# Kernel optimization log

Hardware: AMD Instinct MI355X
Metric: run time of the kernel (lower is better)

The kernel has to match this reference:

```python
import jax, jax.numpy as jnp
import numpy as np

LIMIT = 0.01  # codebook init range, per module's `limit` arg


def setup_inputs() -> dict:
    key = jax.random.key(0)
    k1, k2 = jax.random.split(key)
    B, T, D, K = 64, 1024, 256, 4096
    x = jax.random.normal(k1, (B, T, D), dtype=jnp.float32)
    # codebook: (embedding_dim, num_embeddings), uniform in [-limit, limit]
    vectors = jax.random.uniform(k2, (D, K), dtype=jnp.float32, minval=-LIMIT, maxval=LIMIT)
    return {"x": x, "vectors": vectors}


def reference(x, vectors):
    D = x.shape[-1]
    flat_x = x.reshape(-1, D)  # (N, D)
    # squared euclidean distances to each codebook vector: (N, K)
    distances = ((flat_x ** 2).sum(axis=1, keepdims=True)
                 - 2.0 * flat_x @ vectors
                 + (vectors ** 2).sum(axis=0, keepdims=True))
    encoding_indices = jnp.argmin(distances, axis=1)  # (N,)
    # gather nearest codebook vectors: vectors.T is (K, D)
    quantized_x = jnp.take(vectors.T, encoding_indices, axis=0).reshape(x.shape)
    dictionary_loss = jnp.mean((jax.lax.stop_gradient(x) - quantized_x) ** 2)
    commitment_loss = jnp.mean((x - jax.lax.stop_gradient(quantized_x)) ** 2)
    # straight-through estimator
    quantized_st = x + jax.lax.stop_gradient(quantized_x - x)
    return (quantized_st, dictionary_loss, commitment_loss,
            encoding_indices.reshape(x.shape[0], -1))
```

## Files before the change

kernel.cpp:

```cpp
#include <hip/hip_runtime.h>
#include <cfloat>

#define NROWS 65536
#define DIM   256
#define KCB   4096
#define NBLK  (NROWS / 64)

typedef __attribute__((ext_vector_type(8))) short bf16x8;
typedef __attribute__((ext_vector_type(4))) float f32x4;
typedef unsigned short ushort;
typedef unsigned int uint;


__device__ __forceinline__ bool better(float v1, int i1, float v2, int i2) {
    return (v1 < v2) || (v1 == v2 && i1 < i2);
}

__device__ __forceinline__ float opaque(float x) {
    asm volatile("" : "+v"(x));
    return x;
}

__device__ __forceinline__ ushort f2bf(float f) {
    uint u = __float_as_uint(f);
    return (ushort)((u + 0x7FFFu + ((u >> 16) & 1u)) >> 16);
}

__device__ __forceinline__ void insert4b(float v[4], int idx[4], float s, int k) {
    if (better(s, k, v[3], idx[3])) {
        if (better(s, k, v[2], idx[2])) {
            v[3] = v[2]; idx[3] = idx[2];
            if (better(s, k, v[1], idx[1])) {
                v[2] = v[1]; idx[2] = idx[1];
                if (better(s, k, v[0], idx[0])) {
                    v[1] = v[0]; idx[1] = idx[0]; v[0] = s; idx[0] = k;
                } else { v[1] = s; idx[1] = k; }
            } else { v[2] = s; idx[2] = k; }
        } else { v[3] = s; idx[3] = k; }
    }
}

__global__ void vq_cref_kernel(const float* __restrict__ v,
                               float* __restrict__ cref) {
    int k = blockIdx.x * blockDim.x + threadIdx.x;
    float t = v[k];
    float c = opaque(t * t);
    for (int d = 1; d < DIM; ++d) {
        t = v[d * KCB + k];
        c = c + opaque(t * t);
    }
    cref[k] = c;
}

__global__ void vq_transpose_kernel(const float* __restrict__ v,
                                    float* __restrict__ vt) {
    __shared__ float tile[32][33];
    int d0 = blockIdx.x * 32;
    int k0 = blockIdx.y * 32;
    int tx = threadIdx.x;
    int ty = threadIdx.y;
    #pragma unroll
    for (int i = 0; i < 32; i += 8)
        tile[ty + i][tx] = v[(d0 + ty + i) * KCB + k0 + tx];
    __syncthreads();
    #pragma unroll
    for (int i = 0; i < 32; i += 8)
        vt[(k0 + ty + i) * DIM + d0 + tx] = tile[tx][ty + i];
}

__global__ __launch_bounds__(256) void vq_pack_kernel(const float* __restrict__ vt,
                                                      ushort* __restrict__ vthp) {
    int t = blockIdx.x * 256 + threadIdx.x;
    int lane = t & 63;
    int dt   = (t >> 6) & 7;
    int g    = t >> 9;
    int row  = g * 16 + (lane & 15);
    int dbase = (dt * 4 + (lane >> 4)) * 8;
    const float* src = vt + (size_t)row * DIM + dbase;
    float4 f0 = *(const float4*)src;
    float4 f1 = *(const float4*)(src + 4);
    int4 p;
    p.x = (int)f2bf(f0.x) | ((int)f2bf(f0.y) << 16);
    p.y = (int)f2bf(f0.z) | ((int)f2bf(f0.w) << 16);
    p.z = (int)f2bf(f1.x) | ((int)f2bf(f1.y) << 16);
    p.w = (int)f2bf(f1.z) | ((int)f2bf(f1.w) << 16);
    *(int4*)(vthp + (size_t)t * 8) = p;
}

__global__ __launch_bounds__(256, 4) void vq_mfma_argmin_kernel(
        const float* __restrict__ x, const ushort* __restrict__ vthp,
        const float* __restrict__ vt, const float* __restrict__ cref,
        float* __restrict__ out_q, float* __restrict__ out_idx,
        float* __restrict__ partial) {
    __shared__ __align__(16) ushort Bk[32 * 64 * 8];

    const int tid  = threadIdx.x;
    const int w    = tid >> 6;
    const int lane = tid & 63;
    const int l15  = lane & 15;
    const int quad = lane >> 4;
    const int row0 = blockIdx.x * 64;

    {
        const int r_ = tid >> 2;
        const int q_ = tid & 3;
        const float* xs = &x[(size_t)(row0 + r_) * DIM + q_ * 64];
        #pragma unroll
        for (int i = 0; i < 8; ++i) {
            float4 f0 = *(const float4*)(xs + i * 8);
            float4 f1 = *(const float4*)(xs + i * 8 + 4);
            int4 p;
            p.x = (int)f2bf(f0.x) | ((int)f2bf(f0.y) << 16);
            p.y = (int)f2bf(f0.z) | ((int)f2bf(f0.w) << 16);
            p.z = (int)f2bf(f1.x) | ((int)f2bf(f1.y) << 16);
            p.w = (int)f2bf(f1.z) | ((int)f2bf(f1.w) << 16);
            int u = q_ * 8 + i;
            *(int4*)&Bk[(u * 64 + r_) * 8] = p;
        }
    }
    __syncthreads();

    float m0[4], m1[4];
    #pragma unroll
    for (int nj = 0; nj < 4; ++nj) { m0[nj] = FLT_MAX; m1[nj] = FLT_MAX; }

    for (int kt = 0; kt < 16; ++kt) {
        f32x4 acc[4][4];
        #pragma unroll
        for (int mi = 0; mi < 4; ++mi)
            #pragma unroll
            for (int nj = 0; nj < 4; ++nj)
                acc[mi][nj] = (f32x4)0.f;

        const ushort* akt = vthp
            + ((size_t)(kt * 16 + w * 4) * 8 * 64 + lane) * 8;

        #pragma unroll 2
        for (int dt = 0; dt < 8; ++dt) {
            bf16x8 af[4], bfr[4];
            #pragma unroll
            for (int mi = 0; mi < 4; ++mi)
                af[mi] = *(const bf16x8*)(akt + mi * 4096 + dt * 512);
            #pragma unroll
            for (int nj = 0; nj < 4; ++nj)
                bfr[nj] = *(const bf16x8*)&Bk[((dt * 4 + quad) * 64 + nj * 16 + l15) * 8];
            #pragma unroll
            for (int mi = 0; mi < 4; ++mi)
                #pragma unroll
                for (int nj = 0; nj < 4; ++nj)
                    acc[mi][nj] = __builtin_amdgcn_mfma_f32_16x16x32_bf16(
                        af[mi], bfr[nj], acc[mi][nj], 0, 0, 0);
        }

        const uint ktb = (uint)(kt << 4);
        float4 cv[4];
        #pragma unroll
        for (int mi = 0; mi < 4; ++mi)
            cv[mi] = *(const float4*)&cref[kt * 256 + w * 64 + mi * 16 + quad * 4];

        #pragma unroll
        for (int nj = 0; nj < 4; ++nj) {
            #pragma unroll
            for (int mi = 0; mi < 4; ++mi) {
                #pragma unroll
                for (int r = 0; r < 4; ++r) {
                    float s = fmaf(-2.f, acc[mi][nj][r], (&cv[mi].x)[r]);
                    uint  pk = (__float_as_uint(s) & 0xFFFFFF00u)
                             | (ktb + (uint)(mi * 4 + r));
                    float f = __uint_as_float(pk);
                    m1[nj] = __builtin_amdgcn_fmed3f(f, m0[nj], m1[nj]);
                    m0[nj] = fminf(m0[nj], f);
                }
            }
        }
    }

    float mv[4][4];
    int   mi_[4][4];
    #pragma unroll
    for (int nj = 0; nj < 4; ++nj) {
        uint b0 = __float_as_uint(m0[nj]);
        uint b1 = __float_as_uint(m1[nj]);
        int id0 = (int)(b0 & 255u);
        int id1 = (int)(b1 & 255u);
        mv[nj][0] = m0[nj];
        mi_[nj][0] = ((id0 >> 4) << 8) + w * 64 + (((id0 >> 2) & 3) << 4)
                   + (quad << 2) + (id0 & 3);
        mv[nj][1] = m1[nj];
        mi_[nj][1] = ((id1 >> 4) << 8) + w * 64 + (((id1 >> 2) & 3) << 4)
                   + (quad << 2) + (id1 & 3);
        mv[nj][2] = FLT_MAX; mi_[nj][2] = 0;
        mv[nj][3] = FLT_MAX; mi_[nj][3] = 0;
    }
    #pragma unroll
    for (int off = 16; off <= 32; off <<= 1) {
        #pragma unroll
        for (int nj = 0; nj < 4; ++nj) {
            float ov[4]; int oi[4];
            #pragma unroll
            for (int s = 0; s < 4; ++s) {
                ov[s] = __shfl_xor(mv[nj][s], off);
                oi[s] = __shfl_xor(mi_[nj][s], off);
            }
            #pragma unroll
            for (int s = 0; s < 4; ++s)
                insert4b(mv[nj], mi_[nj], ov[s], oi[s]);
        }
    }

    __syncthreads();
    float2* mbuf  = (float2*)Bk;
    int*    candL = (int*)(Bk + 8192);
    int*    kwin  = (int*)(Bk + 8704);
    float*  rsum  = (float*)(Bk + 8960);
    if (quad == 0) {
        #pragma unroll
        for (int nj = 0; nj < 4; ++nj) {
            int row_local = nj * 16 + l15;
            #pragma unroll
            for (int s = 0; s < 4; ++s)
                mbuf[row_local * 16 + w * 4 + s] =
                    make_float2(mv[nj][s], __int_as_float(mi_[nj][s]));
        }
    }
    __syncthreads();
    if (tid < 64) {
        float bv[4] = {FLT_MAX, FLT_MAX, FLT_MAX, FLT_MAX};
        int   bi[4] = {0, 0, 0, 0};
        #pragma unroll
        for (int j = 0; j < 16; ++j) {
            float2 p = mbuf[tid * 16 + j];
            insert4b(bv, bi, p.x, __float_as_int(p.y));
        }
        #pragma unroll
        for (int s = 0; s < 4; ++s)
            candL[tid * 4 + s] = bi[s];
    }
    __syncthreads();

    {
        const int row = tid >> 2;
        const int cl  = tid & 3;
        const int c   = candL[row * 4 + cl];

        const float4* xr = (const float4*)(x + (size_t)(row0 + row) * DIM);
        const float4* vr = (const float4*)(vt + (size_t)c * DIM);

        float b = 0.f;
        float A_half[2];
        #pragma unroll
        for (int h = 0; h < 2; ++h) {
            float r[8];
            for (int i = 0; i < 16; ++i) {
                float4 xa = xr[h * 32 + i * 2];
                float4 xb = xr[h * 32 + i * 2 + 1];
                float4 va = vr[h * 32 + i * 2];
                float4 vb = vr[h * 32 + i * 2 + 1];
                float xs[8] = {xa.x, xa.y, xa.z, xa.w, xb.x, xb.y, xb.z, xb.w};
                float vs[8] = {va.x, va.y, va.z, va.w, vb.x, vb.y, vb.z, vb.w};
                if (i == 0) {
                    #pragma unroll
                    for (int j = 0; j < 8; ++j) {
                        r[j] = opaque(xs[j] * xs[j]);
                        b = fmaf(2.f * xs[j], vs[j], b);
                    }
                } else {
                    #pragma unroll
                    for (int j = 0; j < 8; ++j) {
                        r[j] = r[j] + opaque(xs[j] * xs[j]);
                        b = fmaf(2.f * xs[j], vs[j], b);
                    }
                }
            }
            A_half[h] = ((r[0] + r[1]) + (r[2] + r[3])) + ((r[4] + r[5]) + (r[6] + r[7]));
        }
        float A = A_half[0] + A_half[1];

        float bd = (A - b) + cref[c];
        int   bk = c;
        #pragma unroll
        for (int off = 1; off <= 2; off <<= 1) {
            float ov = __shfl_xor(bd, off);
            int   oi = __shfl_xor(bk, off);
            if (better(ov, oi, bd, bk)) { bd = ov; bk = oi; }
        }
        if (cl == 0) {
            kwin[row] = bk;
            out_idx[row0 + row] = (float)bk;
        }
    }
    __syncthreads();

    {
        const int row = tid >> 2;
        const int cl  = tid & 3;
        const int k   = kwin[row];
        const float* xs = x  + (size_t)(row0 + row) * DIM + cl * 64;
        const float* vs = vt + (size_t)k * DIM + cl * 64;
        float*       qs = out_q + (size_t)(row0 + row) * DIM + cl * 64;
        float lsum = 0.f;
        #pragma unroll
        for (int i = 0; i < 16; ++i) {
            float4 xv = *(const float4*)(xs + i * 4);
            float4 qv = *(const float4*)(vs + i * 4);
            *(float4*)(qs + i * 4) = qv;
            float dx = xv.x - qv.x, dy = xv.y - qv.y;
            float dz = xv.z - qv.z, dw = xv.w - qv.w;
            lsum += dx * dx + dy * dy + dz * dz + dw * dw;
        }
        lsum += __shfl_xor(lsum, 1);
        lsum += __shfl_xor(lsum, 2);
        if (cl == 0) rsum[row] = lsum;
    }
    __syncthreads();
    if (tid < 64) {
        float s = rsum[tid];
        #pragma unroll
        for (int off = 32; off > 0; off >>= 1)
            s += __shfl_xor(s, off);
        if (tid == 0) partial[blockIdx.x] = s;
    }
}

__global__ void vq_finalize_kernel(const float* __restrict__ partial,
                                   float* __restrict__ out_loss) {
    __shared__ double sd[256];
    double s = 0.0;
    for (int i = threadIdx.x; i < NBLK; i += 256)
        s += (double)partial[i];
    sd[threadIdx.x] = s;
    __syncthreads();
    for (int off = 128; off > 0; off >>= 1) {
        if (threadIdx.x < off) sd[threadIdx.x] += sd[threadIdx.x + off];
        __syncthreads();
    }
    if (threadIdx.x == 0) {
        double m = sd[0] / (double)((long long)NROWS * DIM);
        out_loss[0] = (float)m;
        out_loss[1] = (float)m;
    }
}

extern "C" void kernel_launch(void* const* d_in, const int* in_sizes, int n_in,
                              void* d_out, int out_size, void* d_ws, size_t ws_size,
                              hipStream_t stream) {
    const float* x = (const float*)d_in[0];
    const float* v = (const float*)d_in[1];

    float* out      = (float*)d_out;
    float* out_q    = out;
    float* out_loss = out + (size_t)NROWS * DIM;
    float* out_idx  = out + (size_t)NROWS * DIM + 2;

    char*   ws      = (char*)d_ws;
    float*  cref    = (float*)ws;
    float*  partial = (float*)(ws + 1081344);
    float*  vt      = (float*)(ws + 1343488);
    ushort* vthp    = (ushort*)(ws + 5537792);

    vq_cref_kernel<<<KCB / 256, 256, 0, stream>>>(v, cref);
    vq_transpose_kernel<<<dim3(DIM / 32, KCB / 32), dim3(32, 8), 0, stream>>>(v, vt);
    vq_pack_kernel<<<512, 256, 0, stream>>>(vt, vthp);
    vq_mfma_argmin_kernel<<<NBLK, 256, 0, stream>>>(x, vthp, vt, cref,
                                                    out_q, out_idx, partial);
    vq_finalize_kernel<<<1, 256, 0, stream>>>(partial, out_loss);
}
```

Baseline: 418.7 us.

## Split MFMA argmin and exact rescoring/quantize epilogue into separate kernels

The fused kernel is split in two. The MFMA argmin kernel now writes its top-4 candidate indices per row to a global workspace buffer. A new kernel rescoring those candidates in fp32, picks the winner, writes the quantized rows and index, and computes per-block loss partials. This is meant to keep the register- and latency-heavy epilogue from occupying the MFMA kernel's slots and tail, in exchange for an extra launch and a candidate round trip through global memory.

```diff
diff --git a/kernel.cpp b/kernel.cpp
--- a/kernel.cpp
+++ b/kernel.cpp
@@ -4,7 +4,6 @@
 #define NROWS 65536
 #define DIM   256
 #define KCB   4096
-#define NBLK  (NROWS / 64)
 
 typedef __attribute__((ext_vector_type(8))) short bf16x8;
 typedef __attribute__((ext_vector_type(4))) float f32x4;
@@ -89,9 +88,7 @@
 
 __global__ __launch_bounds__(256, 4) void vq_mfma_argmin_kernel(
         const float* __restrict__ x, const ushort* __restrict__ vthp,
-        const float* __restrict__ vt, const float* __restrict__ cref,
-        float* __restrict__ out_q, float* __restrict__ out_idx,
-        float* __restrict__ partial) {
+        const float* __restrict__ cref, int4* __restrict__ cand) {
     __shared__ __align__(16) ushort Bk[32 * 64 * 8];
 
     const int tid  = threadIdx.x;
@@ -209,10 +206,7 @@
     }
 
     __syncthreads();
-    float2* mbuf  = (float2*)Bk;
-    int*    candL = (int*)(Bk + 8192);
-    int*    kwin  = (int*)(Bk + 8704);
-    float*  rsum  = (float*)(Bk + 8960);
+    float2* mbuf = (float2*)Bk;
     if (quad == 0) {
         #pragma unroll
         for (int nj = 0; nj < 4; ++nj) {
@@ -232,72 +226,69 @@
             float2 p = mbuf[tid * 16 + j];
             insert4b(bv, bi, p.x, __float_as_int(p.y));
         }
-        #pragma unroll
-        for (int s = 0; s < 4; ++s)
-            candL[tid * 4 + s] = bi[s];
-    }
-    __syncthreads();
-
-    {
-        const int row = tid >> 2;
-        const int cl  = tid & 3;
-        const int c   = candL[row * 4 + cl];
-
-        const float4* xr = (const float4*)(x + (size_t)(row0 + row) * DIM);
-        const float4* vr = (const float4*)(vt + (size_t)c * DIM);
-
-        float b = 0.f;
-        float A_half[2];
-        #pragma unroll
-        for (int h = 0; h < 2; ++h) {
-            float r[8];
-            for (int i = 0; i < 16; ++i) {
-                float4 xa = xr[h * 32 + i * 2];
-                float4 xb = xr[h * 32 + i * 2 + 1];
-                float4 va = vr[h * 32 + i * 2];
-                float4 vb = vr[h * 32 + i * 2 + 1];
-                float xs[8] = {xa.x, xa.y, xa.z, xa.w, xb.x, xb.y, xb.z, xb.w};
-                float vs[8] = {va.x, va.y, va.z, va.w, vb.x, vb.y, vb.z, vb.w};
-                if (i == 0) {
-                    #pragma unroll
-                    for (int j = 0; j < 8; ++j) {
-                        r[j] = opaque(xs[j] * xs[j]);
-                        b = fmaf(2.f * xs[j], vs[j], b);
-                    }
-                } else {
-                    #pragma unroll
-                    for (int j = 0; j < 8; ++j) {
-                        r[j] = r[j] + opaque(xs[j] * xs[j]);
-                        b = fmaf(2.f * xs[j], vs[j], b);
-                    }
+        cand[row0 + tid] = make_int4(bi[0], bi[1], bi[2], bi[3]);
+    }
+}
+
+__global__ __launch_bounds__(256) void vq_emuquant_kernel(
+        const float* __restrict__ x, const float* __restrict__ vt,
+        const float* __restrict__ cref, const int4* __restrict__ cand,
+        float* __restrict__ out_q, float* __restrict__ out_idx,
+        float* __restrict__ partial) {
+    __shared__ float rsum[64];
+
+    int gid = blockIdx.x * blockDim.x + threadIdx.x;
+    int row = gid >> 2;
+    int cl  = gid & 3;
+    int c   = ((const int*)cand)[gid];
+
+    const float4* xr = (const float4*)(x + (size_t)row * DIM);
+    const float4* vr = (const float4*)(vt + (size_t)c * DIM);
+
+    float b = 0.f;
+    float A_half[2];
+    #pragma unroll
+    for (int h = 0; h < 2; ++h) {
+        float r[8];
+        for (int i = 0; i < 16; ++i) {
+            float4 xa = xr[h * 32 + i * 2];
+            float4 xb = xr[h * 32 + i * 2 + 1];
+            float4 va = vr[h * 32 + i * 2];
+            float4 vb = vr[h * 32 + i * 2 + 1];
+            float xs[8] = {xa.x, xa.y, xa.z, xa.w, xb.x, xb.y, xb.z, xb.w};
+            float vs[8] = {va.x, va.y, va.z, va.w, vb.x, vb.y, vb.z, vb.w};
+            if (i == 0) {
+                #pragma unroll
+                for (int j = 0; j < 8; ++j) {
+                    r[j] = opaque(xs[j] * xs[j]);
+                    b = fmaf(2.f * xs[j], vs[j], b);
+                }
+            } else {
+                #pragma unroll
+                for (int j = 0; j < 8; ++j) {
+                    r[j] = r[j] + opaque(xs[j] * xs[j]);
+                    b = fmaf(2.f * xs[j], vs[j], b);
                 }
             }
-            A_half[h] = ((r[0] + r[1]) + (r[2] + r[3])) + ((r[4] + r[5]) + (r[6] + r[7]));
-        }
-        float A = A_half[0] + A_half[1];
-
-        float bd = (A - b) + cref[c];
-        int   bk = c;
-        #pragma unroll
-        for (int off = 1; off <= 2; off <<= 1) {
-            float ov = __shfl_xor(bd, off);
-            int   oi = __shfl_xor(bk, off);
-            if (better(ov, oi, bd, bk)) { bd = ov; bk = oi; }
-        }
-        if (cl == 0) {
-            kwin[row] = bk;
-            out_idx[row0 + row] = (float)bk;
-        }
-    }
-    __syncthreads();
+        }
+        A_half[h] = ((r[0] + r[1]) + (r[2] + r[3])) + ((r[4] + r[5]) + (r[6] + r[7]));
+    }
+    float A = A_half[0] + A_half[1];
+
+    float bd = (A - b) + cref[c];
+    int   bk = c;
+    #pragma unroll
+    for (int off = 1; off <= 2; off <<= 1) {
+        float ov = __shfl_xor(bd, off);
+        int   oi = __shfl_xor(bk, off);
+        if (better(ov, oi, bd, bk)) { bd = ov; bk = oi; }
+    }
+    if (cl == 0) out_idx[row] = (float)bk;
 
     {
-        const int row = tid >> 2;
-        const int cl  = tid & 3;
-        const int k   = kwin[row];
-        const float* xs = x  + (size_t)(row0 + row) * DIM + cl * 64;
-        const float* vs = vt + (size_t)k * DIM + cl * 64;
-        float*       qs = out_q + (size_t)(row0 + row) * DIM + cl * 64;
+        const float* xs = x     + (size_t)row * DIM + cl * 64;
+        const float* vs = vt    + (size_t)bk  * DIM + cl * 64;
+        float*       qs = out_q + (size_t)row * DIM + cl * 64;
         float lsum = 0.f;
         #pragma unroll
         for (int i = 0; i < 16; ++i) {
@@ -310,15 +301,15 @@
         }
         lsum += __shfl_xor(lsum, 1);
         lsum += __shfl_xor(lsum, 2);
-        if (cl == 0) rsum[row] = lsum;
-    }
-    __syncthreads();
-    if (tid < 64) {
-        float s = rsum[tid];
+        if (cl == 0) rsum[threadIdx.x >> 2] = lsum;
+    }
+    __syncthreads();
+    if (threadIdx.x < 64) {
+        float s = rsum[threadIdx.x];
         #pragma unroll
         for (int off = 32; off > 0; off >>= 1)
             s += __shfl_xor(s, off);
-        if (tid == 0) partial[blockIdx.x] = s;
+        if (threadIdx.x == 0) partial[blockIdx.x] = s;
     }
 }
 
@@ -326,7 +317,7 @@
                                    float* __restrict__ out_loss) {
     __shared__ double sd[256];
     double s = 0.0;
-    for (int i = threadIdx.x; i < NBLK; i += 256)
+    for (int i = threadIdx.x; i < 1024; i += 256)
         s += (double)partial[i];
     sd[threadIdx.x] = s;
     __syncthreads();
@@ -354,6 +345,7 @@
 
     char*   ws      = (char*)d_ws;
     float*  cref    = (float*)ws;
+    int4*   cand    = (int4*)(ws + 32768);
     float*  partial = (float*)(ws + 1081344);
     float*  vt      = (float*)(ws + 1343488);
     ushort* vthp    = (ushort*)(ws + 5537792);
@@ -361,7 +353,8 @@
     vq_cref_kernel<<<KCB / 256, 256, 0, stream>>>(v, cref);
     vq_transpose_kernel<<<dim3(DIM / 32, KCB / 32), dim3(32, 8), 0, stream>>>(v, vt);
     vq_pack_kernel<<<512, 256, 0, stream>>>(vt, vthp);
-    vq_mfma_argmin_kernel<<<NBLK, 256, 0, stream>>>(x, vthp, vt, cref,
-                                                    out_q, out_idx, partial);
+    vq_mfma_argmin_kernel<<<NROWS / 64, 256, 0, stream>>>(x, vthp, cref, cand);
+    vq_emuquant_kernel<<<NROWS * 4 / 256, 256, 0, stream>>>(x, vt, cref, cand,
+                                                            out_q, out_idx, partial);
     vq_finalize_kernel<<<1, 256, 0, stream>>>(partial, out_loss);
 }
```

Result: no change. 416.6 us (-0.5%).
